# Kernel tuning notes

Measured on AMD Instinct MI355X. Metric: run time of the kernel, lower is better.

## Reference

```python
import jax, jax.numpy as jnp
import numpy as np

NUM_BINS = 15


def setup_inputs() -> dict:
    key = jax.random.key(0)
    k1, k2 = jax.random.split(key)
    N, C = 524288, 200
    logits = jax.random.normal(k1, (N, C), dtype=jnp.float32)
    targs = jax.random.randint(k2, (N,), 0, C, dtype=jnp.int64)
    return {"logits": logits, "targs": targs}


def reference(logits, targs):
    # probs, confidences, predictions
    probs = jax.nn.softmax(logits, axis=1)
    confidences = jnp.max(probs, axis=1)            # [N]
    predictions = jnp.argmax(probs, axis=1)         # [N]
    accuracies = (predictions == targs).astype(jnp.float32)

    n = confidences.shape[0]
    # Torch bins: bin b covers (b/NB, (b+1)/NB]  (gt lower, le upper).
    # ceil(conf*NB)-1 maps conf into that half-open-from-below bin.
    bin_idx = jnp.clip(
        jnp.ceil(confidences * NUM_BINS).astype(jnp.int32) - 1, 0, NUM_BINS - 1
    )

    cnt = jax.ops.segment_sum(jnp.ones_like(confidences), bin_idx, num_segments=NUM_BINS)
    conf_sum = jax.ops.segment_sum(confidences, bin_idx, num_segments=NUM_BINS)
    acc_sum = jax.ops.segment_sum(accuracies, bin_idx, num_segments=NUM_BINS)

    safe_cnt = jnp.maximum(cnt, 1.0)
    gap = jnp.abs(conf_sum / safe_cnt - acc_sum / safe_cnt)      # |avg_conf - acc| per bin
    prop = cnt / n                                               # weight of each bin
    ece = jnp.sum(jnp.where(cnt > 0, gap * prop, 0.0))
    return ece.reshape(1)
```

## Files before the change

### kernel.cpp

```cpp
#include <hip/hip_runtime.h>

#define NUM_BINS 15
#define NCOLS 200
#define BLOCK 256
#define LANES_PER_ROW 8
#define ROWS_PER_BLOCK_ITER (BLOCK / LANES_PER_ROW)
#define GRID 1024
#define NREP 16

__device__ __forceinline__ float max4(float4 q) {
    return fmaxf(fmaxf(q.x, q.y), fmaxf(q.z, q.w));
}
__device__ __forceinline__ float exp4sum(float4 q, float m) {
    return __expf(q.x - m) + __expf(q.y - m) + __expf(q.z - m) + __expf(q.w - m);
}

__global__ __launch_bounds__(BLOCK) void ece_main_kernel(
    const float* __restrict__ logits,
    const int* __restrict__ targs,
    double* __restrict__ g_conf,
    unsigned int* __restrict__ g_cnt,
    unsigned int* __restrict__ g_acc,
    int N)
{
    __shared__ float s_conf[NUM_BINS];
    __shared__ unsigned int s_cnt[NUM_BINS];
    __shared__ unsigned int s_acc[NUM_BINS];

    const int t = threadIdx.x;
    if (t < NUM_BINS) { s_conf[t] = 0.0f; s_cnt[t] = 0u; s_acc[t] = 0u; }
    __syncthreads();

    const int lrow = t >> 3;
    const int sub = t & 7;
    const int stride = GRID * ROWS_PER_BLOCK_ITER;

    int row = blockIdx.x * ROWS_PER_BLOCK_ITER + lrow;

    int tg = 0;
    if (sub == 0 && row < N) tg = targs[row];

    for (; row < N; row += stride) {
        const float* rp = logits + (size_t)row * NCOLS + sub * 4;

        float4 q0 = *reinterpret_cast<const float4*>(rp);
        float4 q1 = *reinterpret_cast<const float4*>(rp + 32);
        float4 q2 = *reinterpret_cast<const float4*>(rp + 64);
        float4 q3 = *reinterpret_cast<const float4*>(rp + 96);
        float4 q4 = *reinterpret_cast<const float4*>(rp + 128);
        float4 q5 = *reinterpret_cast<const float4*>(rp + 160);
        const bool has7 = (sub < 2);
        float4 q6 = make_float4(-INFINITY, -INFINITY, -INFINITY, -INFINITY);
        if (has7) q6 = *reinterpret_cast<const float4*>(rp + 192);

        float tl = 0.0f;
        int tg_next = 0;
        if (sub == 0) {
            tl = logits[(size_t)row * NCOLS + tg];
            int rn = row + stride;
            if (rn < N) tg_next = targs[rn];
        }

        float m = fmaxf(fmaxf(max4(q0), max4(q1)),
                        fmaxf(fmaxf(max4(q2), max4(q3)),
                              fmaxf(max4(q4), max4(q5))));
        if (has7) m = fmaxf(m, max4(q6));
        m = fmaxf(m, __shfl_xor(m, 1));
        m = fmaxf(m, __shfl_xor(m, 2));
        m = fmaxf(m, __shfl_xor(m, 4));

        float s = exp4sum(q0, m) + exp4sum(q1, m) + exp4sum(q2, m)
                + exp4sum(q3, m) + exp4sum(q4, m) + exp4sum(q5, m);
        if (has7) s += exp4sum(q6, m);
        s += __shfl_xor(s, 1);
        s += __shfl_xor(s, 2);
        s += __shfl_xor(s, 4);

        if (sub == 0) {
            float conf = 1.0f / s;
            int b = (int)ceilf(conf * (float)NUM_BINS) - 1;
            b = min(max(b, 0), NUM_BINS - 1);
            atomicAdd(&s_conf[b], conf);
            atomicAdd(&s_cnt[b], 1u);
            if (tl == m) atomicAdd(&s_acc[b], 1u);
        }
        tg = tg_next;
    }

    __syncthreads();
    if (t < NUM_BINS) {
        unsigned int c = s_cnt[t];
        if (c > 0u) {
            const int rep = blockIdx.x & (NREP - 1);
            atomicAdd(&g_cnt[rep * NUM_BINS + t], c);
            atomicAdd(&g_acc[rep * NUM_BINS + t], s_acc[t]);
            atomicAdd(&g_conf[rep * NUM_BINS + t], (double)s_conf[t]);
        }
    }
}

__global__ void ece_final_kernel(
    const double* __restrict__ g_conf,
    const unsigned int* __restrict__ g_cnt,
    const unsigned int* __restrict__ g_acc,
    float* __restrict__ out,
    int N)
{
    const int t = threadIdx.x;
    float part = 0.0f;
    if (t < NUM_BINS) {
        double conf = 0.0;
        unsigned long long cnt = 0, acc = 0;
        #pragma unroll
        for (int r = 0; r < NREP; ++r) {
            conf += g_conf[r * NUM_BINS + t];
            cnt  += g_cnt[r * NUM_BINS + t];
            acc  += g_acc[r * NUM_BINS + t];
        }
        if (cnt > 0) {
            double dc = (double)cnt;
            double gap = fabs(conf / dc - (double)acc / dc);
            part = (float)(gap * (dc / (double)N));
        }
    }
    #pragma unroll
    for (int off = 32; off > 0; off >>= 1) part += __shfl_xor(part, off);
    if (t == 0) out[0] = part;
}

extern "C" void kernel_launch(void* const* d_in, const int* in_sizes, int n_in,
                              void* d_out, int out_size, void* d_ws, size_t ws_size,
                              hipStream_t stream) {
    const float* logits = (const float*)d_in[0];
    const int* targs = (const int*)d_in[1];
    const int N = in_sizes[1];

    double* g_conf = (double*)d_ws;
    unsigned int* g_cnt = (unsigned int*)(g_conf + NREP * NUM_BINS);
    unsigned int* g_acc = g_cnt + NREP * NUM_BINS;
    const size_t ws_used = NREP * NUM_BINS * (sizeof(double) + 2 * sizeof(unsigned int));

    hipMemsetAsync(d_ws, 0, ws_used, stream);

    const int total_groups = (N + ROWS_PER_BLOCK_ITER - 1) / ROWS_PER_BLOCK_ITER;
    const int grid = min(total_groups, GRID);
    ece_main_kernel<<<grid, BLOCK, 0, stream>>>(logits, targs, g_conf, g_cnt, g_acc, N);
    ece_final_kernel<<<1, 64, 0, stream>>>(g_conf, g_cnt, g_acc, (float*)d_out, N);
}
```

Baseline: 85.04 us.

## Fuse main and final ECE kernels via cooperative grid sync

Replaces the memset, the main kernel and the final-reduction kernel with one cooperative kernel. Each block writes its per-bin partials to its own slot, so no global atomics or memset are needed, then grid.sync() lets block 0 reduce them. This removes two launches and the memset, at the cost of a grid-wide barrier and a serial final reduction over up to 1024 blocks per bin. The grid size is derived from occupancy times 256 CUs, and the old two-kernel path is kept as a fallback.

```diff
diff --git a/kernel.cpp b/kernel.cpp
--- a/kernel.cpp
+++ b/kernel.cpp
@@ -1,11 +1,13 @@
 #include <hip/hip_runtime.h>
+#include <hip/hip_cooperative_groups.h>
+
+namespace cg = cooperative_groups;
 
 #define NUM_BINS 15
 #define NCOLS 200
 #define BLOCK 256
-#define LANES_PER_ROW 8
-#define ROWS_PER_BLOCK_ITER (BLOCK / LANES_PER_ROW)
-#define GRID 1024
+#define MAXGRID 1024
+#define RPI 32
 #define NREP 16
 
 __device__ __forceinline__ float max4(float4 q) {
@@ -15,28 +17,17 @@
     return __expf(q.x - m) + __expf(q.y - m) + __expf(q.z - m) + __expf(q.w - m);
 }
 
-__global__ __launch_bounds__(BLOCK) void ece_main_kernel(
-    const float* __restrict__ logits,
-    const int* __restrict__ targs,
-    double* __restrict__ g_conf,
-    unsigned int* __restrict__ g_cnt,
-    unsigned int* __restrict__ g_acc,
-    int N)
-{
-    __shared__ float s_conf[NUM_BINS];
-    __shared__ unsigned int s_cnt[NUM_BINS];
-    __shared__ unsigned int s_acc[NUM_BINS];
-
-    const int t = threadIdx.x;
-    if (t < NUM_BINS) { s_conf[t] = 0.0f; s_cnt[t] = 0u; s_acc[t] = 0u; }
-    __syncthreads();
-
+__device__ __forceinline__ void ece_block_accum(
+    const float* __restrict__ logits, const int* __restrict__ targs,
+    int N, int nblk,
+    float* s_conf, unsigned int* s_cnt, unsigned int* s_acc)
+{
+    const int t = threadIdx.x;
     const int lrow = t >> 3;
     const int sub = t & 7;
-    const int stride = GRID * ROWS_PER_BLOCK_ITER;
-
-    int row = blockIdx.x * ROWS_PER_BLOCK_ITER + lrow;
-
+    const int stride = nblk * RPI;
+
+    int row = blockIdx.x * RPI + lrow;
     int tg = 0;
     if (sub == 0 && row < N) tg = targs[row];
 
@@ -86,6 +77,90 @@
         }
         tg = tg_next;
     }
+}
+
+__global__ __launch_bounds__(BLOCK, 4) void ece_fused_kernel(
+    const float* __restrict__ logits,
+    const int* __restrict__ targs,
+    float* __restrict__ g_conf,
+    unsigned int* __restrict__ g_cnt,
+    unsigned int* __restrict__ g_acc,
+    float* __restrict__ out,
+    int N, int nblk)
+{
+    __shared__ float s_conf[NUM_BINS];
+    __shared__ unsigned int s_cnt[NUM_BINS];
+    __shared__ unsigned int s_acc[NUM_BINS];
+    __shared__ double s_term[NUM_BINS];
+
+    const int t = threadIdx.x;
+    if (t < NUM_BINS) { s_conf[t] = 0.0f; s_cnt[t] = 0u; s_acc[t] = 0u; }
+    __syncthreads();
+
+    ece_block_accum(logits, targs, N, nblk, s_conf, s_cnt, s_acc);
+
+    __syncthreads();
+    if (t < NUM_BINS) {
+        __hip_atomic_store(&g_conf[t * nblk + blockIdx.x], s_conf[t],
+                           __ATOMIC_RELAXED, __HIP_MEMORY_SCOPE_AGENT);
+        __hip_atomic_store(&g_cnt[t * nblk + blockIdx.x], s_cnt[t],
+                           __ATOMIC_RELAXED, __HIP_MEMORY_SCOPE_AGENT);
+        __hip_atomic_store(&g_acc[t * nblk + blockIdx.x], s_acc[t],
+                           __ATOMIC_RELAXED, __HIP_MEMORY_SCOPE_AGENT);
+    }
+
+    cg::this_grid().sync();
+
+    if (blockIdx.x == 0) {
+        const int b = t >> 4, k = t & 15;
+        double conf = 0.0; unsigned int cnt = 0u, acc = 0u;
+        if (b < NUM_BINS) {
+            for (int blk = k; blk < nblk; blk += 16) {
+                conf += (double)__hip_atomic_load(&g_conf[b * nblk + blk],
+                            __ATOMIC_RELAXED, __HIP_MEMORY_SCOPE_AGENT);
+                cnt += __hip_atomic_load(&g_cnt[b * nblk + blk],
+                            __ATOMIC_RELAXED, __HIP_MEMORY_SCOPE_AGENT);
+                acc += __hip_atomic_load(&g_acc[b * nblk + blk],
+                            __ATOMIC_RELAXED, __HIP_MEMORY_SCOPE_AGENT);
+            }
+            #pragma unroll
+            for (int off = 1; off <= 8; off <<= 1) {
+                conf += __shfl_xor(conf, off);
+                cnt  += __shfl_xor(cnt, off);
+                acc  += __shfl_xor(acc, off);
+            }
+            if (k == 0) {
+                double term = 0.0;
+                if (cnt > 0u) {
+                    double dc = (double)cnt;
+                    term = fabs(conf / dc - (double)acc / dc) * (dc / (double)N);
+                }
+                s_term[b] = term;
+            }
+        }
+        __syncthreads();
+        if (t == 0) {
+            double e = 0.0;
+            #pragma unroll
+            for (int b2 = 0; b2 < NUM_BINS; ++b2) e += s_term[b2];
+            out[0] = (float)e;
+        }
+    }
+}
+
+__global__ __launch_bounds__(BLOCK) void ece_main_kernel(
+    const float* __restrict__ logits, const int* __restrict__ targs,
+    double* __restrict__ g_conf, unsigned int* __restrict__ g_cnt,
+    unsigned int* __restrict__ g_acc, int N, int nblk)
+{
+    __shared__ float s_conf[NUM_BINS];
+    __shared__ unsigned int s_cnt[NUM_BINS];
+    __shared__ unsigned int s_acc[NUM_BINS];
+    const int t = threadIdx.x;
+    if (t < NUM_BINS) { s_conf[t] = 0.0f; s_cnt[t] = 0u; s_acc[t] = 0u; }
+    __syncthreads();
+
+    ece_block_accum(logits, targs, N, nblk, s_conf, s_cnt, s_acc);
 
     __syncthreads();
     if (t < NUM_BINS) {
@@ -100,11 +175,8 @@
 }
 
 __global__ void ece_final_kernel(
-    const double* __restrict__ g_conf,
-    const unsigned int* __restrict__ g_cnt,
-    const unsigned int* __restrict__ g_acc,
-    float* __restrict__ out,
-    int N)
+    const double* __restrict__ g_conf, const unsigned int* __restrict__ g_cnt,
+    const unsigned int* __restrict__ g_acc, float* __restrict__ out, int N)
 {
     const int t = threadIdx.x;
     float part = 0.0f;
@@ -119,8 +191,7 @@
         }
         if (cnt > 0) {
             double dc = (double)cnt;
-            double gap = fabs(conf / dc - (double)acc / dc);
-            part = (float)(gap * (dc / (double)N));
+            part = (float)(fabs(conf / dc - (double)acc / dc) * (dc / (double)N));
         }
     }
     #pragma unroll
@@ -133,17 +204,33 @@
                               hipStream_t stream) {
     const float* logits = (const float*)d_in[0];
     const int* targs = (const int*)d_in[1];
-    const int N = in_sizes[1];
-
-    double* g_conf = (double*)d_ws;
-    unsigned int* g_cnt = (unsigned int*)(g_conf + NREP * NUM_BINS);
-    unsigned int* g_acc = g_cnt + NREP * NUM_BINS;
-    const size_t ws_used = NREP * NUM_BINS * (sizeof(double) + 2 * sizeof(unsigned int));
-
-    hipMemsetAsync(d_ws, 0, ws_used, stream);
-
-    const int total_groups = (N + ROWS_PER_BLOCK_ITER - 1) / ROWS_PER_BLOCK_ITER;
-    const int grid = min(total_groups, GRID);
-    ece_main_kernel<<<grid, BLOCK, 0, stream>>>(logits, targs, g_conf, g_cnt, g_acc, N);
-    ece_final_kernel<<<1, 64, 0, stream>>>(g_conf, g_cnt, g_acc, (float*)d_out, N);
-}
+    int N = in_sizes[1];
+    float* out = (float*)d_out;
+
+    int occ = 0;
+    hipError_t oe = hipOccupancyMaxActiveBlocksPerMultiprocessor(
+        &occ, ece_fused_kernel, BLOCK, 0);
+    int nblk = (oe == hipSuccess) ? occ * 256 : 0;
+    if (nblk > MAXGRID) nblk = MAXGRID;
+    const size_t ws_need = (size_t)NUM_BINS * MAXGRID * (4 + 4 + 4);
+
+    if (nblk >= 256 && ws_size >= ws_need) {
+        float* g_conf = (float*)d_ws;
+        unsigned int* g_cnt = (unsigned int*)(g_conf + NUM_BINS * nblk);
+        unsigned int* g_acc = g_cnt + NUM_BINS * nblk;
+        void* args[] = { &logits, &targs, &g_conf, &g_cnt, &g_acc,
+                         &out, &N, &nblk };
+        hipLaunchCooperativeKernel((void*)ece_fused_kernel,
+                                   dim3(nblk), dim3(BLOCK), args, 0, stream);
+    } else {
+        double* g_conf = (double*)d_ws;
+        unsigned int* g_cnt = (unsigned int*)(g_conf + NREP * NUM_BINS);
+        unsigned int* g_acc = g_cnt + NREP * NUM_BINS;
+        const size_t ws_used = NREP * NUM_BINS * (sizeof(double) + 8);
+        hipMemsetAsync(d_ws, 0, ws_used, stream);
+        const int grid = MAXGRID;
+        ece_main_kernel<<<grid, BLOCK, 0, stream>>>(logits, targs, g_conf,
+                                                    g_cnt, g_acc, N, grid);
+        ece_final_kernel<<<1, 64, 0, stream>>>(g_conf, g_cnt, g_acc, out, N);
+    }
+}
```

New measurement: 230.2 us. 171% more time.
